# Performance work log

Measured on AMD Instinct MI355X. Metric: run time of the kernel, lower is better.

The kernel has to match this reference:

```python
import jax, jax.numpy as jnp
import numpy as np

B, L, D, V = 32, 2048, 768, 32000


def setup_inputs() -> dict:
    key = jax.random.key(0)
    k1, k2, k3, k4 = jax.random.split(key, 4)
    last_hidden_states = jax.random.normal(k1, (B, L, D), dtype=jnp.float32)
    attention_mask = jax.random.randint(k2, (B, L), 0, 2, dtype=jnp.int32)
    input_ids = jax.random.randint(k3, (B, L), 0, V, dtype=jnp.int64)
    idf_lookup = jax.random.uniform(k4, (V,), dtype=jnp.float32)  # learned/loaded IDF table
    alpha = jnp.float32(1.0)
    return {
        "last_hidden_states": last_hidden_states,
        "attention_mask": attention_mask,
        "input_ids": input_ids,
        "idf_lookup": idf_lookup,
        "alpha": alpha,
    }


def reference(last_hidden_states, attention_mask, input_ids, idf_lookup, alpha):
    dtype = last_hidden_states.dtype
    maskf = attention_mask.astype(dtype)                       # [B, L]
    # Per-row histogram over vocab (vectorized equivalent of torch.unique counts)
    rows = jnp.arange(B)[:, None]                              # [B, 1]
    hist = jnp.zeros((B, V), dtype=dtype).at[rows, input_ids].add(maskf)  # [B, V]
    counts = jnp.take_along_axis(hist, input_ids, axis=1)      # [B, L] count of each token in its row
    n_valid = maskf.sum(axis=1, keepdims=True)                 # [B, 1]
    tf = counts / jnp.maximum(n_valid, 1.0)                    # term frequency
    idf = jnp.take(idf_lookup, input_ids, axis=0).astype(dtype)  # [B, L]
    weights = (1.0 + alpha.astype(dtype) * tf * idf) * maskf   # [B, L]
    norm = jnp.maximum(weights.sum(axis=1, keepdims=True), 1e-12)
    pooled = jnp.einsum("bld,bl->bd", last_hidden_states, weights) / norm  # [B, D]
    return pooled
```

## Files before the change

kernel.cpp:

```cpp
#include <hip/hip_runtime.h>

#define BB 32
#define LL 2048
#define DD 768
#define VV 32000
#define NSEG 32

__global__ __launch_bounds__(512) void weights_kernel(
    const int* __restrict__ ids, const int* __restrict__ mask,
    const float* __restrict__ idf, const float* __restrict__ alpha_p,
    float* __restrict__ wc, int* __restrict__ lc,
    int* __restrict__ nv_ws, float* __restrict__ inv_ws,
    float* __restrict__ out)
{
    __shared__ unsigned int hist[VV / 2];
    __shared__ int   wtot[8];
    __shared__ float wsum_s[8];

    const int tid  = threadIdx.x;
    const int lane = tid & 63, wave = tid >> 6;
    const int b    = blockIdx.x;

    for (int k = tid; k < DD; k += 512) out[b * DD + k] = 0.0f;

    for (int i = tid; i < VV / 2; i += 512) hist[i] = 0u;

    const int4 ia = ((const int4*)(ids  + b * LL))[tid];
    const int4 ma = ((const int4*)(mask + b * LL))[tid];
    const int idv[4] = {ia.x, ia.y, ia.z, ia.w};
    const int mv[4]  = {ma.x, ma.y, ma.z, ma.w};

    float idfv[4];
    #pragma unroll
    for (int k = 0; k < 4; ++k) idfv[k] = idf[idv[k]];

    __syncthreads();

    int c_t = 0;
    #pragma unroll
    for (int k = 0; k < 4; ++k) {
        if (mv[k]) {
            atomicAdd(&hist[idv[k] >> 1], 1u << ((idv[k] & 1) * 16));
            c_t++;
        }
    }

    int incl = c_t;
    #pragma unroll
    for (int off = 1; off < 64; off <<= 1) {
        const int n = __shfl_up(incl, off, 64);
        if (lane >= off) incl += n;
    }
    if (lane == 63) wtot[wave] = incl;
    __syncthreads();

    int wpre = 0, total_valid = 0;
    #pragma unroll
    for (int w = 0; w < 8; ++w) {
        const int t = wtot[w];
        if (w < wave) wpre += t;
        total_valid += t;
    }
    const int excl = wpre + incl - c_t;

    const float nvf   = fmaxf((float)total_valid, 1.0f);
    const float alpha = alpha_p[0];

    float wsum = 0.0f;
    float wv[4];
    #pragma unroll
    for (int k = 0; k < 4; ++k) {
        const int id       = idv[k];
        const unsigned raw = hist[id >> 1];
        const int cnt      = (raw >> ((id & 1) * 16)) & 0xffff;
        const float tf     = (float)cnt / nvf;
        const float w      = (1.0f + alpha * tf * idfv[k]) * (float)(mv[k] != 0);
        wv[k] = w;
        wsum += w;
    }

    int pos = b * LL + excl;
    #pragma unroll
    for (int k = 0; k < 4; ++k) {
        if (mv[k]) { wc[pos] = wv[k]; lc[pos] = tid * 4 + k; pos++; }
    }

    #pragma unroll
    for (int off = 32; off; off >>= 1) wsum += __shfl_down(wsum, off, 64);
    if (lane == 0) wsum_s[wave] = wsum;
    __syncthreads();
    if (tid == 0) {
        float t = 0.0f;
        #pragma unroll
        for (int w = 0; w < 8; ++w) t += wsum_s[w];
        inv_ws[b] = 1.0f / fmaxf(t, 1e-12f);
        nv_ws[b]  = total_valid;
    }
}

__global__ __launch_bounds__(256) void pool_kernel(
    const float* __restrict__ h, const float* __restrict__ wc,
    const int* __restrict__ lc, const int* __restrict__ nv_ws,
    const float* __restrict__ inv_ws, float* __restrict__ out)
{
    __shared__ float w_s[64];
    __shared__ int   l_s[64];
    __shared__ float red[4 * DD];

    const int tid  = threadIdx.x;
    const int wave = tid >> 6, lane = tid & 63;
    const int b = blockIdx.y, s = blockIdx.x;

    const int nv    = nv_ws[b];
    const int chunk = (nv + NSEG - 1) / NSEG;
    const int lo    = s * chunk;
    const int cnt   = max(0, min(lo + chunk, nv) - lo);

    if (tid < cnt) {
        w_s[tid] = wc[b * LL + lo + tid];
        l_s[tid] = lc[b * LL + lo + tid];
    }
    __syncthreads();

    const float* hb = h + (size_t)b * (LL * DD);
    float4 a0 = {0,0,0,0}, a1 = {0,0,0,0}, a2 = {0,0,0,0};

    int i = wave;
    for (; i + 4 < cnt; i += 8) {
        const float wA = w_s[i],     wB = w_s[i + 4];
        const float4* pA = (const float4*)(hb + (size_t)l_s[i]     * DD);
        const float4* pB = (const float4*)(hb + (size_t)l_s[i + 4] * DD);
        const float4 vA0 = pA[lane], vA1 = pA[64 + lane], vA2 = pA[128 + lane];
        const float4 vB0 = pB[lane], vB1 = pB[64 + lane], vB2 = pB[128 + lane];
        a0.x = fmaf(vA0.x, wA, a0.x); a0.y = fmaf(vA0.y, wA, a0.y);
        a0.z = fmaf(vA0.z, wA, a0.z); a0.w = fmaf(vA0.w, wA, a0.w);
        a1.x = fmaf(vA1.x, wA, a1.x); a1.y = fmaf(vA1.y, wA, a1.y);
        a1.z = fmaf(vA1.z, wA, a1.z); a1.w = fmaf(vA1.w, wA, a1.w);
        a2.x = fmaf(vA2.x, wA, a2.x); a2.y = fmaf(vA2.y, wA, a2.y);
        a2.z = fmaf(vA2.z, wA, a2.z); a2.w = fmaf(vA2.w, wA, a2.w);
        a0.x = fmaf(vB0.x, wB, a0.x); a0.y = fmaf(vB0.y, wB, a0.y);
        a0.z = fmaf(vB0.z, wB, a0.z); a0.w = fmaf(vB0.w, wB, a0.w);
        a1.x = fmaf(vB1.x, wB, a1.x); a1.y = fmaf(vB1.y, wB, a1.y);
        a1.z = fmaf(vB1.z, wB, a1.z); a1.w = fmaf(vB1.w, wB, a1.w);
        a2.x = fmaf(vB2.x, wB, a2.x); a2.y = fmaf(vB2.y, wB, a2.y);
        a2.z = fmaf(vB2.z, wB, a2.z); a2.w = fmaf(vB2.w, wB, a2.w);
    }
    for (; i < cnt; i += 4) {
        const float w = w_s[i];
        const float4* p = (const float4*)(hb + (size_t)l_s[i] * DD);
        const float4 v0 = p[lane], v1 = p[64 + lane], v2 = p[128 + lane];
        a0.x = fmaf(v0.x, w, a0.x); a0.y = fmaf(v0.y, w, a0.y);
        a0.z = fmaf(v0.z, w, a0.z); a0.w = fmaf(v0.w, w, a0.w);
        a1.x = fmaf(v1.x, w, a1.x); a1.y = fmaf(v1.y, w, a1.y);
        a1.z = fmaf(v1.z, w, a1.z); a1.w = fmaf(v1.w, w, a1.w);
        a2.x = fmaf(v2.x, w, a2.x); a2.y = fmaf(v2.y, w, a2.y);
        a2.z = fmaf(v2.z, w, a2.z); a2.w = fmaf(v2.w, w, a2.w);
    }

    float4* r = (float4*)(red + wave * DD);
    r[lane] = a0; r[64 + lane] = a1; r[128 + lane] = a2;
    __syncthreads();

    const float inv = inv_ws[b];
    for (int k = tid; k < DD; k += 256) {
        const float v = red[k] + red[DD + k] + red[2 * DD + k] + red[3 * DD + k];
        atomicAdd(&out[b * DD + k], v * inv);
    }
}

extern "C" void kernel_launch(void* const* d_in, const int* in_sizes, int n_in,
                              void* d_out, int out_size, void* d_ws, size_t ws_size,
                              hipStream_t stream)
{
    const float* h     = (const float*)d_in[0];
    const int*   mask  = (const int*)  d_in[1];
    const int*   ids   = (const int*)  d_in[2];
    const float* idf   = (const float*)d_in[3];
    const float* alpha = (const float*)d_in[4];
    float*       out   = (float*)d_out;

    float* wc  = (float*)d_ws;
    int*   lc  = (int*)(wc + BB * LL);
    int*   nv  = lc + BB * LL;
    float* inv = (float*)(nv + BB);

    weights_kernel<<<BB, 512, 0, stream>>>(ids, mask, idf, alpha, wc, lc, nv, inv, out);
    pool_kernel<<<dim3(NSEG, BB), 256, 0, stream>>>(h, wc, lc, nv, inv, out);
}
```

Measured before the change: 263.3 us.

## Split pooling over column slices instead of token segments, drop atomics

The pooling kernel now gives each block a 32-column slice of D and all valid tokens of a batch row, rather than a segment of tokens across all 768 columns. Partial sums are reduced with wave shuffles and shared memory, and each block writes its output directly, so the output zeroing and global atomics go away. Each row read is now only 128 bytes per token (8 lanes per row, 32 rows in flight per block), which can reduce coalescing efficiency. Every block also reloads all compacted weights and indices into shared memory (16KB).

After: 265.8 us. Within noise of the previous version (+1.0%).

```diff
diff --git a/kernel.cpp b/kernel.cpp
--- a/kernel.cpp
+++ b/kernel.cpp
@@ -4,14 +4,14 @@
 #define LL 2048
 #define DD 768
 #define VV 32000
-#define NSEG 32
+#define COLS 32
+#define DSEG (DD / COLS)
 
 __global__ __launch_bounds__(512) void weights_kernel(
     const int* __restrict__ ids, const int* __restrict__ mask,
     const float* __restrict__ idf, const float* __restrict__ alpha_p,
     float* __restrict__ wc, int* __restrict__ lc,
-    int* __restrict__ nv_ws, float* __restrict__ inv_ws,
-    float* __restrict__ out)
+    int* __restrict__ nv_ws, float* __restrict__ inv_ws)
 {
     __shared__ unsigned int hist[VV / 2];
     __shared__ int   wtot[8];
@@ -20,8 +20,6 @@
     const int tid  = threadIdx.x;
     const int lane = tid & 63, wave = tid >> 6;
     const int b    = blockIdx.x;
-
-    for (int k = tid; k < DD; k += 512) out[b * DD + k] = 0.0f;
 
     for (int i = tid; i < VV / 2; i += 512) hist[i] = 0u;
 
@@ -98,73 +96,78 @@
     }
 }
 
+__device__ __forceinline__ void fma4(float4& acc, const float4 v, const float s)
+{
+    acc.x = fmaf(v.x, s, acc.x);
+    acc.y = fmaf(v.y, s, acc.y);
+    acc.z = fmaf(v.z, s, acc.z);
+    acc.w = fmaf(v.w, s, acc.w);
+}
+
 __global__ __launch_bounds__(256) void pool_kernel(
     const float* __restrict__ h, const float* __restrict__ wc,
     const int* __restrict__ lc, const int* __restrict__ nv_ws,
     const float* __restrict__ inv_ws, float* __restrict__ out)
 {
-    __shared__ float w_s[64];
-    __shared__ int   l_s[64];
-    __shared__ float red[4 * DD];
+    __shared__ float  w_s[LL];
+    __shared__ int    l_s[LL];
+    __shared__ float4 red4[4][8];
 
     const int tid  = threadIdx.x;
     const int wave = tid >> 6, lane = tid & 63;
-    const int b = blockIdx.y, s = blockIdx.x;
+    const int b    = blockIdx.y;
+    const int c0   = blockIdx.x * COLS;
 
-    const int nv    = nv_ws[b];
-    const int chunk = (nv + NSEG - 1) / NSEG;
-    const int lo    = s * chunk;
-    const int cnt   = max(0, min(lo + chunk, nv) - lo);
-
-    if (tid < cnt) {
-        w_s[tid] = wc[b * LL + lo + tid];
-        l_s[tid] = lc[b * LL + lo + tid];
+    const int nv = nv_ws[b];
+    for (int i = tid; i < nv; i += 256) {
+        w_s[i] = wc[b * LL + i];
+        l_s[i] = lc[b * LL + i];
     }
     __syncthreads();
 
-    const float* hb = h + (size_t)b * (LL * DD);
-    float4 a0 = {0,0,0,0}, a1 = {0,0,0,0}, a2 = {0,0,0,0};
+    const float* hb = h + (size_t)b * (LL * DD) + c0 + (lane & 7) * 4;
+    const int g = wave * 8 + (lane >> 3);
 
-    int i = wave;
-    for (; i + 4 < cnt; i += 8) {
-        const float wA = w_s[i],     wB = w_s[i + 4];
-        const float4* pA = (const float4*)(hb + (size_t)l_s[i]     * DD);
-        const float4* pB = (const float4*)(hb + (size_t)l_s[i + 4] * DD);
-        const float4 vA0 = pA[lane], vA1 = pA[64 + lane], vA2 = pA[128 + lane];
-        const float4 vB0 = pB[lane], vB1 = pB[64 + lane], vB2 = pB[128 + lane];
-        a0.x = fmaf(vA0.x, wA, a0.x); a0.y = fmaf(vA0.y, wA, a0.y);
-        a0.z = fmaf(vA0.z, wA, a0.z); a0.w = fmaf(vA0.w, wA, a0.w);
-        a1.x = fmaf(vA1.x, wA, a1.x); a1.y = fmaf(vA1.y, wA, a1.y);
-        a1.z = fmaf(vA1.z, wA, a1.z); a1.w = fmaf(vA1.w, wA, a1.w);
-        a2.x = fmaf(vA2.x, wA, a2.x); a2.y = fmaf(vA2.y, wA, a2.y);
-        a2.z = fmaf(vA2.z, wA, a2.z); a2.w = fmaf(vA2.w, wA, a2.w);
-        a0.x = fmaf(vB0.x, wB, a0.x); a0.y = fmaf(vB0.y, wB, a0.y);
-        a0.z = fmaf(vB0.z, wB, a0.z); a0.w = fmaf(vB0.w, wB, a0.w);
-        a1.x = fmaf(vB1.x, wB, a1.x); a1.y = fmaf(vB1.y, wB, a1.y);
-        a1.z = fmaf(vB1.z, wB, a1.z); a1.w = fmaf(vB1.w, wB, a1.w);
-        a2.x = fmaf(vB2.x, wB, a2.x); a2.y = fmaf(vB2.y, wB, a2.y);
-        a2.z = fmaf(vB2.z, wB, a2.z); a2.w = fmaf(vB2.w, wB, a2.w);
+    float4 acc = {0.f, 0.f, 0.f, 0.f};
+    int t = g;
+    for (; t + 96 < nv; t += 128) {
+        const float wA = w_s[t];      const int lA = l_s[t];
+        const float wB = w_s[t + 32]; const int lB = l_s[t + 32];
+        const float wC = w_s[t + 64]; const int lC = l_s[t + 64];
+        const float wD = w_s[t + 96]; const int lD = l_s[t + 96];
+        const float4 vA = *(const float4*)(hb + (size_t)lA * DD);
+        const float4 vB = *(const float4*)(hb + (size_t)lB * DD);
+        const float4 vC = *(const float4*)(hb + (size_t)lC * DD);
+        const float4 vD = *(const float4*)(hb + (size_t)lD * DD);
+        fma4(acc, vA, wA); fma4(acc, vB, wB);
+        fma4(acc, vC, wC); fma4(acc, vD, wD);
     }
-    for (; i < cnt; i += 4) {
-        const float w = w_s[i];
-        const float4* p = (const float4*)(hb + (size_t)l_s[i] * DD);
-        const float4 v0 = p[lane], v1 = p[64 + lane], v2 = p[128 + lane];
-        a0.x = fmaf(v0.x, w, a0.x); a0.y = fmaf(v0.y, w, a0.y);
-        a0.z = fmaf(v0.z, w, a0.z); a0.w = fmaf(v0.w, w, a0.w);
-        a1.x = fmaf(v1.x, w, a1.x); a1.y = fmaf(v1.y, w, a1.y);
-        a1.z = fmaf(v1.z, w, a1.z); a1.w = fmaf(v1.w, w, a1.w);
-        a2.x = fmaf(v2.x, w, a2.x); a2.y = fmaf(v2.y, w, a2.y);
-        a2.z = fmaf(v2.z, w, a2.z); a2.w = fmaf(v2.w, w, a2.w);
+    for (; t < nv; t += 32) {
+        const float w = w_s[t]; const int l = l_s[t];
+        const float4 v = *(const float4*)(hb + (size_t)l * DD);
+        fma4(acc, v, w);
     }
 
-    float4* r = (float4*)(red + wave * DD);
-    r[lane] = a0; r[64 + lane] = a1; r[128 + lane] = a2;
+    #pragma unroll
+    for (int off = 8; off < 64; off <<= 1) {
+        acc.x += __shfl_xor(acc.x, off, 64);
+        acc.y += __shfl_xor(acc.y, off, 64);
+        acc.z += __shfl_xor(acc.z, off, 64);
+        acc.w += __shfl_xor(acc.w, off, 64);
+    }
+    if (lane < 8) red4[wave][lane] = acc;
     __syncthreads();
 
-    const float inv = inv_ws[b];
-    for (int k = tid; k < DD; k += 256) {
-        const float v = red[k] + red[DD + k] + red[2 * DD + k] + red[3 * DD + k];
-        atomicAdd(&out[b * DD + k], v * inv);
+    if (tid < 8) {
+        const float4 r0 = red4[0][tid], r1 = red4[1][tid];
+        const float4 r2 = red4[2][tid], r3 = red4[3][tid];
+        const float inv = inv_ws[b];
+        float4 r;
+        r.x = (r0.x + r1.x + r2.x + r3.x) * inv;
+        r.y = (r0.y + r1.y + r2.y + r3.y) * inv;
+        r.z = (r0.z + r1.z + r2.z + r3.z) * inv;
+        r.w = (r0.w + r1.w + r2.w + r3.w) * inv;
+        ((float4*)(out + b * DD + c0))[tid] = r;
     }
 }
 
@@ -184,6 +187,6 @@
     int*   nv  = lc + BB * LL;
     float* inv = (float*)(nv + BB);
 
-    weights_kernel<<<BB, 512, 0, stream>>>(ids, mask, idf, alpha, wc, lc, nv, inv, out);
-    pool_kernel<<<dim3(NSEG, BB), 256, 0, stream>>>(h, wc, lc, nv, inv, out);
+    weights_kernel<<<BB, 512, 0, stream>>>(ids, mask, idf, alpha, wc, lc, nv, inv);
+    pool_kernel<<<dim3(DSEG, BB), 256, 0, stream>>>(h, wc, lc, nv, inv, out);
 }
```
